# Kernel tuning notes

Measured on AMD Instinct MI355X. Metric: run time of the kernel, lower is better.

## Reference

```python
import jax, jax.numpy as jnp
import numpy as np

B, S, D = 4, 1024, 1024
H, G = 16, 8            # num_heads, num_query_groups
HD = D // H             # head_dim = 64
E, TOPK, ED = 8, 2, 2 * D   # experts, top_k, expert_dim
GH = D // 2             # gate hidden
EPS = 1e-5


def setup_inputs() -> dict:
    key = jax.random.key(0)
    ks = iter(jax.random.split(key, 32))
    rn = lambda shape, s=0.02: jax.random.normal(next(ks), shape, jnp.float32) * s
    return {
        "x": jax.random.normal(next(ks), (B, S, D), jnp.float32),
        # GQA projections (stored [in, out])
        "wq": rn((D, G * HD)), "bq": jnp.zeros((G * HD,), jnp.float32),
        "wk": rn((D, D)), "bk": jnp.zeros((D,), jnp.float32),
        "wv": rn((D, D)), "bv": jnp.zeros((D,), jnp.float32),
        "wo": rn((D, D)), "bo": jnp.zeros((D,), jnp.float32),
        # LayerNorms
        "ln1_g": jnp.ones((D,), jnp.float32), "ln1_b": jnp.zeros((D,), jnp.float32),
        "ln2_g": jnp.ones((D,), jnp.float32), "ln2_b": jnp.zeros((D,), jnp.float32),
        # MoE gate: Linear(D, D//2) -> ReLU -> Linear(D//2, E)
        "gw1": rn((D, GH)), "gb1": jnp.zeros((GH,), jnp.float32),
        "gw2": rn((GH, E)), "gb2": jnp.zeros((E,), jnp.float32),
        # stacked expert FFNs: Linear(D, ED) -> GELU -> Linear(ED, D)
        "ew1": rn((E, D, ED)), "eb1": jnp.zeros((E, ED), jnp.float32),
        "ew2": rn((E, ED, D)), "eb2": jnp.zeros((E, D), jnp.float32),
    }


def _layernorm(x, g, b):
    mu = jnp.mean(x, axis=-1, keepdims=True)
    var = jnp.var(x, axis=-1, keepdims=True)
    return (x - mu) * jax.lax.rsqrt(var + EPS) * g + b


def _block(x, wq, bq, wk, bk, wv, bv, wo, bo, ln1_g, ln1_b, ln2_g, ln2_b,
           gw1, gb1, gw2, gb2, ew1, eb1, ew2, eb2):
    # --- GQA self-attention (dropout is identity in eval) ---
    h = _layernorm(x, ln1_g, ln1_b)
    q = (h @ wq + bq).reshape(B, S, G, HD).transpose(0, 2, 1, 3)   # [B,G,S,hd]
    k = (h @ wk + bk).reshape(B, S, H, HD).transpose(0, 2, 1, 3)   # [B,H,S,hd]
    v = (h @ wv + bv).reshape(B, S, H, HD).transpose(0, 2, 1, 3)
    q = jnp.repeat(q, H // G, axis=1)                              # repeat_interleave -> [B,H,S,hd]
    scores = jnp.einsum("bhqd,bhkd->bhqk", q, k) * (HD ** -0.5)
    attn = jax.nn.softmax(scores, axis=-1)
    ao = jnp.einsum("bhqk,bhkd->bhqd", attn, v)
    ao = ao.transpose(0, 2, 1, 3).reshape(B, S, D) @ wo + bo
    x = x + ao

    # --- MoE FFN ---
    h2 = _layernorm(x, ln2_g, ln2_b).reshape(-1, D)                # [T,D], T=B*S
    gate_logits = jax.nn.relu(h2 @ gw1 + gb1) @ gw2 + gb2          # [T,E]
    gate_w = jax.nn.softmax(gate_logits, axis=-1)
    top_w, top_i = jax.lax.top_k(gate_w, TOPK)                     # [T,k]
    top_w = jax.nn.softmax(top_w, axis=-1)                         # renormalize among top-k
    combine = jnp.sum(jax.nn.one_hot(top_i, E, dtype=h2.dtype) * top_w[..., None], axis=1)  # [T,E]
    hid = jax.nn.gelu(jnp.einsum("td,edh->teh", h2, ew1) + eb1, approximate=False)          # [T,E,ED]
    expert_out = jnp.einsum("teh,ehd->ted", hid, ew2) + eb2        # [T,E,D]
    moe = jnp.einsum("ted,te->td", expert_out, combine).reshape(B, S, D)
    return x + moe


def reference(x, wq, bq, wk, bk, wv, bv, wo, bo, ln1_g, ln1_b, ln2_g, ln2_b,
              gw1, gb1, gw2, gb2, ew1, eb1, ew2, eb2):
    return _block(x, wq, bq, wk, bk, wv, bv, wo, bo, ln1_g, ln1_b, ln2_g, ln2_b,
                  gw1, gb1, gw2, gb2, ew1, eb1, ew2, eb2)
```

## Files before the change

### kernel.cpp

```cpp
#include <hip/hip_runtime.h>

typedef __bf16 bf16x8 __attribute__((ext_vector_type(8)));
typedef float f32x4 __attribute__((ext_vector_type(4)));
typedef unsigned int u32x4 __attribute__((ext_vector_type(4)));
typedef unsigned int u32x2 __attribute__((ext_vector_type(2)));

#define DEV static __device__ __forceinline__

DEV unsigned short f2bf(float f) {
  unsigned int u = __builtin_bit_cast(unsigned int, f);
  u += 0x7fffu + ((u >> 16) & 1u);
  return (unsigned short)(u >> 16);
}
DEV float bf2f(unsigned int hbits) { return __builtin_bit_cast(float, hbits << 16); }

DEV bf16x8 load_bf8(const unsigned short* p) {
  u32x4 u = *(const u32x4*)p;
  return __builtin_bit_cast(bf16x8, u);
}
DEV void unpack8(u32x4 u, float f[8]) {
  f[0] = bf2f(u.x & 0xffffu); f[1] = bf2f(u.x >> 16);
  f[2] = bf2f(u.y & 0xffffu); f[3] = bf2f(u.y >> 16);
  f[4] = bf2f(u.z & 0xffffu); f[5] = bf2f(u.z >> 16);
  f[6] = bf2f(u.w & 0xffffu); f[7] = bf2f(u.w >> 16);
}
DEV void gload_lds16(const void* g, void* l) {
  __builtin_amdgcn_global_load_lds((const __attribute__((address_space(1))) void*)g,
                                   (__attribute__((address_space(3))) void*)l, 16, 0, 0);
}
DEV f32x4 mfma16(bf16x8 a, bf16x8 b, f32x4 c) {
  return __builtin_amdgcn_mfma_f32_16x16x32_bf16(a, b, c, 0, 0, 0);
}

__global__ __launch_bounds__(256) void cm_transpose(
    const float* __restrict__ src, unsigned short* __restrict__ dst,
    int K, int N, long srcStrideE, long dstStrideE) {
  src += (long)blockIdx.z * srcStrideE;
  dst += (long)blockIdx.z * dstStrideE;
  __shared__ float t[32][33];
  const int n0 = blockIdx.x * 32, k0 = blockIdx.y * 32;
  const int tx = threadIdx.x & 31, ty = threadIdx.x >> 5;
#pragma unroll
  for (int j = 0; j < 4; ++j) {
    int k = k0 + ty + j * 8, n = n0 + tx;
    if (k < K && n < N) t[ty + j * 8][tx] = src[(long)k * N + n];
  }
  __syncthreads();
#pragma unroll
  for (int j = 0; j < 4; ++j) {
    int n = n0 + ty + j * 8, k = k0 + tx;
    if (n < N && k < K) dst[(long)n * K + k] = f2bf(t[tx][ty + j * 8]);
  }
}

__global__ __launch_bounds__(256) void cm_transpose_split(
    const float* __restrict__ src, unsigned short* __restrict__ dhi,
    unsigned short* __restrict__ dlo, int K, int N) {
  __shared__ float t[32][33];
  const int n0 = blockIdx.x * 32, k0 = blockIdx.y * 32;
  const int tx = threadIdx.x & 31, ty = threadIdx.x >> 5;
#pragma unroll
  for (int j = 0; j < 4; ++j) {
    int k = k0 + ty + j * 8, n = n0 + tx;
    if (k < K && n < N) t[ty + j * 8][tx] = src[(long)k * N + n];
  }
  __syncthreads();
#pragma unroll
  for (int j = 0; j < 4; ++j) {
    int n = n0 + ty + j * 8, k = k0 + tx;
    if (n < N && k < K) {
      float v = t[tx][ty + j * 8];
      unsigned short hi = f2bf(v);
      dhi[(long)n * K + k] = hi;
      dlo[(long)n * K + k] = f2bf(v - bf2f(hi));
    }
  }
}

template <bool WLO>
__global__ __launch_bounds__(256) void cm_ln(
    const float* __restrict__ x, const float* __restrict__ g, const float* __restrict__ b,
    unsigned short* __restrict__ ob, unsigned short* __restrict__ olo) {
  const int row = blockIdx.x, tid = threadIdx.x;
  const f32x4 v = *(const f32x4*)(x + (long)row * 1024 + tid * 4);
  float s1 = v[0] + v[1] + v[2] + v[3];
  float s2 = v[0] * v[0] + v[1] * v[1] + v[2] * v[2] + v[3] * v[3];
#pragma unroll
  for (int m = 32; m >= 1; m >>= 1) { s1 += __shfl_xor(s1, m); s2 += __shfl_xor(s2, m); }
  __shared__ float r1[4], r2[4];
  if ((tid & 63) == 0) { r1[tid >> 6] = s1; r2[tid >> 6] = s2; }
  __syncthreads();
  s1 = r1[0] + r1[1] + r1[2] + r1[3];
  s2 = r2[0] + r2[1] + r2[2] + r2[3];
  const float mean = s1 * (1.f / 1024.f);
  const float rs = rsqrtf(s2 * (1.f / 1024.f) - mean * mean + 1e-5f);
  const f32x4 gg = *(const f32x4*)(g + tid * 4);
  const f32x4 bb = *(const f32x4*)(b + tid * 4);
  float o[4];
  unsigned short hi[4];
#pragma unroll
  for (int i = 0; i < 4; ++i) {
    o[i] = (v[i] - mean) * rs * gg[i] + bb[i];
    hi[i] = f2bf(o[i]);
  }
  u32x2 pk;
  pk.x = (unsigned)hi[0] | ((unsigned)hi[1] << 16);
  pk.y = (unsigned)hi[2] | ((unsigned)hi[3] << 16);
  *(u32x2*)(ob + (long)row * 1024 + tid * 4) = pk;
  if (WLO) {
    u32x2 pl;
    pl.x = (unsigned)f2bf(o[0] - bf2f(hi[0])) | ((unsigned)f2bf(o[1] - bf2f(hi[1])) << 16);
    pl.y = (unsigned)f2bf(o[2] - bf2f(hi[2])) | ((unsigned)f2bf(o[3] - bf2f(hi[3])) << 16);
    *(u32x2*)(olo + (long)row * 1024 + tid * 4) = pl;
  }
}

enum { EP_BF16 = 0, EP_RELU = 1, EP_GELU = 2, EP_RES_F32 = 3 };

template <int EPI, int MODE>
__global__ __launch_bounds__(256, 2) void cm_gemm_bt(
    const unsigned short* __restrict__ A, int lda,
    const unsigned short* __restrict__ BT, long btStrideE, int ldb,
    const float* __restrict__ bias, int biasStrideE,
    const float* __restrict__ res,
    void* __restrict__ outp, int ldc,
    int M, int K,
    const int* __restrict__ cnt, const int* __restrict__ offs,
    const int* __restrict__ rowidx) {
  const int gx = gridDim.x, gy = gridDim.y;
  const int nwg = gx * gy * (int)gridDim.z;
  int flat = (int)blockIdx.x + gx * ((int)blockIdx.y + gy * (int)blockIdx.z);
  {
    const int q = nwg >> 3, r = nwg & 7, xcd = flat & 7, idx = flat >> 3;
    flat = (xcd < r ? xcd * (q + 1) : r * (q + 1) + (xcd - r) * q) + idx;
  }
  const int bx = flat % gx;
  const int rest = flat / gx;
  const int by = rest % gy;
  const int z = rest / gy;

  int valid = M, rowbase = 0;
  const unsigned short* Bp = BT;
  const float* biasp = bias;
  if (MODE > 0) {
    valid = cnt[z];
    if (by * 128 >= valid) return;
    rowbase = offs[z];
    Bp += (long)z * btStrideE;
    biasp += (long)z * biasStrideE;
  }
  const int tid = threadIdx.x;
  const int brow = by * 128, bcol = bx * 128;
  const int wid = tid >> 6, lane = tid & 63;
  const int wr = wid >> 1, wc = wid & 1;
  const int srow0 = tid >> 2, scol = (tid & 3) * 8;

  __shared__ __align__(16) unsigned short As[128 * 32];
  __shared__ __align__(16) unsigned short Bs[128 * 32];

  long asrc[2], bsrc[2];
#pragma unroll
  for (int i = 0; i < 2; ++i) {
    int m = brow + srow0 + i * 64;
    if (MODE == 0) {
      asrc[i] = (long)m * lda;
    } else {
      int p = m < valid ? m : valid - 1;
      if (MODE == 1) asrc[i] = (long)rowidx[z * 4096 + p] * lda;
      else           asrc[i] = (long)(rowbase + p) * lda;
    }
    bsrc[i] = (long)(bcol + srow0 + i * 64) * ldb;
  }

  f32x4 acc[4][4] = {};

  for (int k0 = 0; k0 < K; k0 += 32) {
#pragma unroll
    for (int i = 0; i < 2; ++i) {
      gload_lds16(A + asrc[i] + k0 + scol, &As[(srow0 + i * 64) * 32 + scol]);
      gload_lds16(Bp + bsrc[i] + k0 + scol, &Bs[(srow0 + i * 64) * 32 + scol]);
    }
    __syncthreads();
    bf16x8 af[4], bfr[4];
#pragma unroll
    for (int m = 0; m < 4; ++m)
      af[m] = load_bf8(&As[(wr * 64 + m * 16 + (lane & 15)) * 32 + (lane >> 4) * 8]);
#pragma unroll
    for (int n = 0; n < 4; ++n)
      bfr[n] = load_bf8(&Bs[(wc * 64 + n * 16 + (lane & 15)) * 32 + (lane >> 4) * 8]);
#pragma unroll
    for (int m = 0; m < 4; ++m)
#pragma unroll
      for (int n = 0; n < 4; ++n)
        acc[m][n] = mfma16(af[m], bfr[n], acc[m][n]);
    __syncthreads();
  }

#pragma unroll
  for (int m = 0; m < 4; ++m) {
#pragma unroll
    for (int rr = 0; rr < 4; ++rr) {
      const int lrow = brow + wr * 64 + m * 16 + (lane >> 4) * 4 + rr;
      if (MODE > 0 && lrow >= valid) continue;
      const long orow = (long)(rowbase + lrow);
#pragma unroll
      for (int n = 0; n < 4; ++n) {
        const int gcol = bcol + wc * 64 + n * 16 + (lane & 15);
        float vv = acc[m][n][rr] + biasp[gcol];
        if constexpr (EPI == EP_RELU) vv = fmaxf(vv, 0.f);
        if constexpr (EPI == EP_GELU) vv = 0.5f * vv * (1.f + erff(vv * 0.70710678f));
        if constexpr (EPI == EP_RES_F32)
          ((float*)outp)[orow * ldc + gcol] = vv + res[orow * ldc + gcol];
        else
          ((unsigned short*)outp)[orow * ldc + gcol] = f2bf(vv);
      }
    }
  }
}

__global__ __launch_bounds__(256, 2) void cm_gemm_gate(
    const unsigned short* __restrict__ Ah, const unsigned short* __restrict__ Al,
    const unsigned short* __restrict__ Bh, const unsigned short* __restrict__ Bl,
    const float* __restrict__ bias, float* __restrict__ C) {
  const int tid = threadIdx.x;
  const int brow = blockIdx.y * 128, bcol = blockIdx.x * 128;
  const int wid = tid >> 6, lane = tid & 63;
  const int wr = wid >> 1, wc = wid & 1;
  const int srow0 = tid >> 2, scol = (tid & 3) * 8;

  __shared__ __align__(16) unsigned short Ash[128 * 32], Asl[128 * 32];
  __shared__ __align__(16) unsigned short Bsh[128 * 32], Bsl[128 * 32];

  f32x4 acc[4][4] = {};

  for (int k0 = 0; k0 < 1024; k0 += 32) {
#pragma unroll
    for (int i = 0; i < 2; ++i) {
      const long ar = (long)(brow + srow0 + i * 64) * 1024 + k0 + scol;
      const long br = (long)(bcol + srow0 + i * 64) * 1024 + k0 + scol;
      const int lo = (srow0 + i * 64) * 32 + scol;
      gload_lds16(Ah + ar, &Ash[lo]);
      gload_lds16(Al + ar, &Asl[lo]);
      gload_lds16(Bh + br, &Bsh[lo]);
      gload_lds16(Bl + br, &Bsl[lo]);
    }
    __syncthreads();
    bf16x8 ah[4], al[4], bh[4], bl[4];
#pragma unroll
    for (int m = 0; m < 4; ++m) {
      const int ro = (wr * 64 + m * 16 + (lane & 15)) * 32 + (lane >> 4) * 8;
      ah[m] = load_bf8(&Ash[ro]); al[m] = load_bf8(&Asl[ro]);
    }
#pragma unroll
    for (int n = 0; n < 4; ++n) {
      const int ro = (wc * 64 + n * 16 + (lane & 15)) * 32 + (lane >> 4) * 8;
      bh[n] = load_bf8(&Bsh[ro]); bl[n] = load_bf8(&Bsl[ro]);
    }
#pragma unroll
    for (int m = 0; m < 4; ++m)
#pragma unroll
      for (int n = 0; n < 4; ++n) {
        acc[m][n] = mfma16(al[m], bh[n], acc[m][n]);
        acc[m][n] = mfma16(ah[m], bl[n], acc[m][n]);
        acc[m][n] = mfma16(ah[m], bh[n], acc[m][n]);
      }
    __syncthreads();
  }

#pragma unroll
  for (int m = 0; m < 4; ++m)
#pragma unroll
    for (int rr = 0; rr < 4; ++rr) {
      const long orow = brow + wr * 64 + m * 16 + (lane >> 4) * 4 + rr;
#pragma unroll
      for (int n = 0; n < 4; ++n) {
        const int gcol = bcol + wc * 64 + n * 16 + (lane & 15);
        C[orow * 512 + gcol] = fmaxf(acc[m][n][rr] + bias[gcol], 0.f);
      }
    }
}

__global__ __launch_bounds__(256) void cm_vtrans(
    const unsigned short* __restrict__ qkv, unsigned short* __restrict__ Vt) {
  const int stile = blockIdx.x, bh = blockIdx.y;
  const int b = bh >> 4, h = bh & 15;
  const int tid = threadIdx.x;
  __shared__ __align__(16) unsigned short t[64][72];
  const int d0 = (tid & 7) * 8, sl = tid >> 3;
#pragma unroll
  for (int i = 0; i < 2; ++i) {
    const int s = sl + i * 32;
    *(u32x4*)&t[s][d0] =
        *(const u32x4*)(qkv + (long)(b * 1024 + stile * 64 + s) * 2560 + 1536 + h * 64 + d0);
  }
  __syncthreads();
  const int s0 = (tid & 7) * 8, dl = tid >> 3;
#pragma unroll
  for (int i = 0; i < 2; ++i) {
    const int d = dl + i * 32;
    unsigned short vals[8];
#pragma unroll
    for (int j = 0; j < 8; ++j) vals[j] = t[s0 + j][d];
    u32x4 u;
    u.x = vals[0] | ((unsigned)vals[1] << 16);
    u.y = vals[2] | ((unsigned)vals[3] << 16);
    u.z = vals[4] | ((unsigned)vals[5] << 16);
    u.w = vals[6] | ((unsigned)vals[7] << 16);
    *(u32x4*)(Vt + (long)(bh * 64 + d) * 1024 + stile * 64 + s0) = u;
  }
}

__global__ __launch_bounds__(256, 2) void cm_attn(
    const unsigned short* __restrict__ qkv,
    const unsigned short* __restrict__ Vt,
    unsigned short* __restrict__ ao) {
  const int qt = blockIdx.x, bh = blockIdx.y;
  const int b = bh >> 4, h = bh & 15, g = h >> 1;
  const int tid = threadIdx.x, wid = tid >> 6, lane = tid & 63;
  const int q0 = qt * 32;

  __shared__ __align__(16) unsigned short sc[32][1032];
  __shared__ float rowrcp[32];

  bf16x8 bq[2][2];
#pragma unroll
  for (int nf = 0; nf < 2; ++nf)
#pragma unroll
    for (int ks = 0; ks < 2; ++ks)
      bq[nf][ks] = load_bf8(qkv + (long)(b * 1024 + q0 + nf * 16 + (lane & 15)) * 2560 +
                            g * 64 + ks * 32 + (lane >> 4) * 8);

#pragma unroll 1
  for (int c = 0; c < 4; ++c) {
    const int kb = wid * 256 + c * 64;
    f32x4 acc[4][2] = {};
#pragma unroll
    for (int ks = 0; ks < 2; ++ks) {
      bf16x8 ak[4];
#pragma unroll
      for (int mf = 0; mf < 4; ++mf)
        ak[mf] = load_bf8(qkv + (long)(b * 1024 + kb + mf * 16 + (lane & 15)) * 2560 +
                          512 + h * 64 + ks * 32 + (lane >> 4) * 8);
#pragma unroll
      for (int mf = 0; mf < 4; ++mf)
#pragma unroll
        for (int nf = 0; nf < 2; ++nf)
          acc[mf][nf] = mfma16(ak[mf], bq[nf][ks], acc[mf][nf]);
    }
#pragma unroll
    for (int mf = 0; mf < 4; ++mf)
#pragma unroll
      for (int nf = 0; nf < 2; ++nf) {
        const int q = nf * 16 + (lane & 15);
        const int key = kb + mf * 16 + (lane >> 4) * 4;
        u32x2 pk;
        pk.x = (unsigned)f2bf(acc[mf][nf][0] * 0.125f) |
               ((unsigned)f2bf(acc[mf][nf][1] * 0.125f) << 16);
        pk.y = (unsigned)f2bf(acc[mf][nf][2] * 0.125f) |
               ((unsigned)f2bf(acc[mf][nf][3] * 0.125f) << 16);
        *(u32x2*)&sc[q][key] = pk;
      }
  }
  __syncthreads();

  {
    const int row = tid >> 3, seg = tid & 7;
    float mx = -1e30f;
#pragma unroll
    for (int i = 0; i < 16; ++i) {
      float f[8];
      unpack8(*(const u32x4*)&sc[row][i * 64 + seg * 8], f);
#pragma unroll
      for (int j = 0; j < 8; ++j) mx = fmaxf(mx, f[j]);
    }
#pragma unroll
    for (int m = 4; m >= 1; m >>= 1) mx = fmaxf(mx, __shfl_xor(mx, m));
    float sum = 0.f;
#pragma unroll 1
    for (int i = 0; i < 16; ++i) {
      float f[8];
      unpack8(*(const u32x4*)&sc[row][i * 64 + seg * 8], f);
      float e[8];
#pragma unroll
      for (int j = 0; j < 8; ++j) { e[j] = __expf(f[j] - mx); sum += e[j]; }
      u32x4 o;
      o.x = (unsigned)f2bf(e[0]) | ((unsigned)f2bf(e[1]) << 16);
      o.y = (unsigned)f2bf(e[2]) | ((unsigned)f2bf(e[3]) << 16);
      o.z = (unsigned)f2bf(e[4]) | ((unsigned)f2bf(e[5]) << 16);
      o.w = (unsigned)f2bf(e[6]) | ((unsigned)f2bf(e[7]) << 16);
      *(u32x4*)&sc[row][i * 64 + seg * 8] = o;
    }
#pragma unroll
    for (int m = 4; m >= 1; m >>= 1) sum += __shfl_xor(sum, m);
    if (seg == 0) rowrcp[row] = 1.f / sum;
  }
  __syncthreads();

  {
    f32x4 acc[2] = {};
    const unsigned short* vtb = Vt + (long)bh * 64 * 1024;
#pragma unroll 4
    for (int k0 = 0; k0 < 1024; k0 += 32) {
      const bf16x8 bv =
          load_bf8(vtb + (long)(wid * 16 + (lane & 15)) * 1024 + k0 + (lane >> 4) * 8);
#pragma unroll
      for (int m = 0; m < 2; ++m) {
        const bf16x8 ap = load_bf8(&sc[m * 16 + (lane & 15)][k0 + (lane >> 4) * 8]);
        acc[m] = mfma16(ap, bv, acc[m]);
      }
    }
#pragma unroll
    for (int m = 0; m < 2; ++m)
#pragma unroll
      for (int rr = 0; rr < 4; ++rr) {
        const int q = m * 16 + (lane >> 4) * 4 + rr;
        const int d = wid * 16 + (lane & 15);
        ao[(long)(b * 1024 + q0 + q) * 1024 + h * 64 + d] = f2bf(acc[m][rr] * rowrcp[q]);
      }
  }
}

__global__ __launch_bounds__(64) void cm_route_pick(
    const float* __restrict__ g1f, const float* __restrict__ gw2, const float* __restrict__ gb2,
    int* __restrict__ pick, int* __restrict__ slot_e, float* __restrict__ rwt) {
  const int t = blockIdx.x, lane = threadIdx.x;
  f32x4 a0 = *(const f32x4*)(g1f + (long)t * 512 + lane * 8);
  f32x4 a1 = *(const f32x4*)(g1f + (long)t * 512 + lane * 8 + 4);
  float logit[8];
#pragma unroll
  for (int e = 0; e < 8; ++e) {
    float s = 0.f;
#pragma unroll
    for (int j = 0; j < 4; ++j) {
      s += a0[j] * gw2[(lane * 8 + j) * 8 + e];
      s += a1[j] * gw2[(lane * 8 + 4 + j) * 8 + e];
    }
#pragma unroll
    for (int m = 32; m >= 1; m >>= 1) s += __shfl_xor(s, m);
    logit[e] = s + gb2[e];
  }
  float mx = logit[0];
#pragma unroll
  for (int e = 1; e < 8; ++e) mx = fmaxf(mx, logit[e]);
  float p[8], sum = 0.f;
#pragma unroll
  for (int e = 0; e < 8; ++e) { p[e] = __expf(logit[e] - mx); sum += p[e]; }
  const float rs = 1.f / sum;
#pragma unroll
  for (int e = 0; e < 8; ++e) p[e] *= rs;
  int i0 = 0;
#pragma unroll
  for (int e = 1; e < 8; ++e) if (p[e] > p[i0]) i0 = e;
  int i1 = (i0 == 0) ? 1 : 0;
#pragma unroll
  for (int e = 0; e < 8; ++e) if (e != i0 && p[e] > p[i1]) i1 = e;
  const float w0 = 1.f / (1.f + __expf(p[i1] - p[i0]));
  if (lane == 0) {
    pick[t] = i0 | (i1 << 8);
    slot_e[t * 2] = i0; slot_e[t * 2 + 1] = i1;
    rwt[t * 2] = w0;    rwt[t * 2 + 1] = 1.f - w0;
  }
}

__global__ __launch_bounds__(256) void cm_route_place(
    const int* __restrict__ pick, int* __restrict__ cnt,
    int* __restrict__ etok, int* __restrict__ slot_p) {
  const int t = blockIdx.x * 256 + threadIdx.x;
  const int lane = threadIdx.x & 63;
  const int pk = pick[t];
  const int p0 = pk & 15, p1 = (pk >> 8) & 15;
  const unsigned long long lt = ((unsigned long long)1 << lane) - 1;
  int my_r0 = 0, my_c0p1 = 0, my_r1 = 0, tot = 0;
#pragma unroll
  for (int e = 0; e < 8; ++e) {
    const unsigned long long m0 = __ballot(p0 == e);
    const unsigned long long m1 = __ballot(p1 == e);
    if (p0 == e) my_r0 = __popcll(m0 & lt);
    if (p1 == e) { my_c0p1 = __popcll(m0); my_r1 = __popcll(m1 & lt); }
    if (lane == e) tot = __popcll(m0) + __popcll(m1);
  }
  int base = 0;
  if (lane < 8 && tot > 0) base = atomicAdd(&cnt[lane], tot);
  const int b0 = __shfl(base, p0);
  const int b1 = __shfl(base, p1);
  const int pos0 = b0 + my_r0;
  const int pos1 = b1 + my_c0p1 + my_r1;
  etok[p0 * 4096 + pos0] = t;
  etok[p1 * 4096 + pos1] = t;
  slot_p[t * 2] = pos0;
  slot_p[t * 2 + 1] = pos1;
}

__global__ void cm_offs(const int* __restrict__ cnt, int* __restrict__ offs) {
  if (threadIdx.x == 0) {
    int s = 0;
#pragma unroll
    for (int e = 0; e < 8; ++e) { offs[e] = s; s += cnt[e]; }
  }
}

__global__ __launch_bounds__(256) void cm_combine(
    const float* __restrict__ x2, const unsigned short* __restrict__ eo,
    const int* __restrict__ slot_e, const int* __restrict__ slot_p,
    const float* __restrict__ rwt, const int* __restrict__ offs,
    float* __restrict__ outp) {
  const int t = blockIdx.x, tid = threadIdx.x;
  const long r0 = (long)(offs[slot_e[t * 2]] + slot_p[t * 2]);
  const long r1 = (long)(offs[slot_e[t * 2 + 1]] + slot_p[t * 2 + 1]);
  const float w0 = rwt[t * 2], w1 = rwt[t * 2 + 1];
  const f32x4 xv = *(const f32x4*)(x2 + (long)t * 1024 + tid * 4);
  u32x2 u0 = *(const u32x2*)(eo + r0 * 1024 + tid * 4);
  u32x2 u1 = *(const u32x2*)(eo + r1 * 1024 + tid * 4);
  f32x4 o;
  o[0] = xv[0] + w0 * bf2f(u0.x & 0xffffu) + w1 * bf2f(u1.x & 0xffffu);
  o[1] = xv[1] + w0 * bf2f(u0.x >> 16) + w1 * bf2f(u1.x >> 16);
  o[2] = xv[2] + w0 * bf2f(u0.y & 0xffffu) + w1 * bf2f(u1.y & 0xffffu);
  o[3] = xv[3] + w0 * bf2f(u0.y >> 16) + w1 * bf2f(u1.y >> 16);
  *(f32x4*)(outp + (long)t * 1024 + tid * 4) = o;
}

extern "C" void kernel_launch(void* const* d_in, const int* in_sizes, int n_in,
                              void* d_out, int out_size, void* d_ws, size_t ws_size,
                              hipStream_t stream) {
  if (n_in < 21) return;
  const float* x    = (const float*)d_in[0];
  const float* wq   = (const float*)d_in[1];
  const float* bq   = (const float*)d_in[2];
  const float* wk   = (const float*)d_in[3];
  const float* bk   = (const float*)d_in[4];
  const float* wv   = (const float*)d_in[5];
  const float* bv   = (const float*)d_in[6];
  const float* wo   = (const float*)d_in[7];
  const float* bo   = (const float*)d_in[8];
  const float* ln1g = (const float*)d_in[9];
  const float* ln1b = (const float*)d_in[10];
  const float* ln2g = (const float*)d_in[11];
  const float* ln2b = (const float*)d_in[12];
  const float* gw1  = (const float*)d_in[13];
  const float* gb1  = (const float*)d_in[14];
  const float* gw2  = (const float*)d_in[15];
  const float* gb2  = (const float*)d_in[16];
  const float* ew1  = (const float*)d_in[17];
  const float* eb1  = (const float*)d_in[18];
  const float* ew2  = (const float*)d_in[19];
  const float* eb2  = (const float*)d_in[20];
  float* outp = (float*)d_out;

  char* ws = (char*)d_ws;
  size_t off = 0;
  auto carve = [&](size_t bytes) -> char* {
    char* p = ws + off;
    off += (bytes + 255) & ~(size_t)255;
    return p;
  };
  unsigned short* wqkvT = (unsigned short*)carve(2560l * 1024 * 2);
  unsigned short* woT   = (unsigned short*)carve(1024l * 1024 * 2);
  unsigned short* gw1hT = (unsigned short*)carve(512l * 1024 * 2);
  unsigned short* gw1lT = (unsigned short*)carve(512l * 1024 * 2);
  unsigned short* ew1T  = (unsigned short*)carve(8l * 2048 * 1024 * 2);
  unsigned short* ew2T  = (unsigned short*)carve(8l * 1024 * 2048 * 2);
  float* bqkv           = (float*)carve(2560 * 4);
  unsigned short* hbuf  = (unsigned short*)carve(4096l * 1024 * 2);
  unsigned short* qkvl  = (unsigned short*)carve(4096l * 2560 * 2);
  unsigned short* Vt    = (unsigned short*)carve(4096l * 1024 * 2);
  unsigned short* ao    = (unsigned short*)carve(4096l * 1024 * 2);
  unsigned short* h2    = (unsigned short*)carve(4096l * 1024 * 2);
  unsigned short* h2lo  = (unsigned short*)carve(4096l * 1024 * 2);
  int* cnt              = (int*)carve(8 * 4);
  int* offs             = (int*)carve(8 * 4);
  int* etok             = (int*)carve(8l * 4096 * 4);
  int* slot_e           = (int*)carve(8192 * 4);
  int* slot_p           = (int*)carve(8192 * 4);
  float* rwt            = (float*)carve(8192 * 4);
  int* pick             = (int*)carve(4096 * 4);
  unsigned short* hid   = (unsigned short*)carve(8192l * 2048 * 2);
  unsigned short* eo    = (unsigned short*)carve(8192l * 1024 * 2);
  if (off > ws_size) return;
  float* x2 = outp;
  float* g1f = (float*)Vt;

  (void)hipMemsetAsync(cnt, 0, 8 * 4, stream);
  (void)hipMemcpyAsync(bqkv, (const void*)bq, 512 * 4, hipMemcpyDeviceToDevice, stream);
  (void)hipMemcpyAsync(bqkv + 512, (const void*)bk, 1024 * 4, hipMemcpyDeviceToDevice, stream);
  (void)hipMemcpyAsync(bqkv + 1536, (const void*)bv, 1024 * 4, hipMemcpyDeviceToDevice, stream);

  cm_transpose<<<dim3(16, 32, 1), 256, 0, stream>>>(wq, wqkvT, 1024, 512, 0l, 0l);
  cm_transpose<<<dim3(32, 32, 1), 256, 0, stream>>>(wk, wqkvT + 512l * 1024, 1024, 1024, 0l, 0l);
  cm_transpose<<<dim3(32, 32, 1), 256, 0, stream>>>(wv, wqkvT + 1536l * 1024, 1024, 1024, 0l, 0l);
  cm_transpose<<<dim3(32, 32, 1), 256, 0, stream>>>(wo, woT, 1024, 1024, 0l, 0l);
  cm_transpose_split<<<dim3(16, 32, 1), 256, 0, stream>>>(gw1, gw1hT, gw1lT, 1024, 512);
  cm_transpose<<<dim3(64, 32, 8), 256, 0, stream>>>(ew1, ew1T, 1024, 2048, 1024l * 2048, 2048l * 1024);
  cm_transpose<<<dim3(32, 64, 8), 256, 0, stream>>>(ew2, ew2T, 2048, 1024, 2048l * 1024, 1024l * 2048);

  cm_ln<false><<<4096, 256, 0, stream>>>(x, ln1g, ln1b, hbuf, nullptr);
  cm_gemm_bt<EP_BF16, 0><<<dim3(20, 32, 1), 256, 0, stream>>>(
      hbuf, 1024, wqkvT, 0l, 1024, bqkv, 0, nullptr, qkvl, 2560, 4096, 1024,
      nullptr, nullptr, nullptr);
  cm_vtrans<<<dim3(16, 64, 1), 256, 0, stream>>>(qkvl, Vt);
  cm_attn<<<dim3(32, 64, 1), 256, 0, stream>>>(qkvl, Vt, ao);
  cm_gemm_bt<EP_RES_F32, 0><<<dim3(8, 32, 1), 256, 0, stream>>>(
      ao, 1024, woT, 0l, 1024, bo, 0, x, x2, 1024, 4096, 1024,
      nullptr, nullptr, nullptr);
  cm_ln<true><<<4096, 256, 0, stream>>>(x2, ln2g, ln2b, h2, h2lo);

  cm_gemm_gate<<<dim3(4, 32, 1), 256, 0, stream>>>(h2, h2lo, gw1hT, gw1lT, gb1, g1f);
  cm_route_pick<<<4096, 64, 0, stream>>>(g1f, gw2, gb2, pick, slot_e, rwt);
  cm_route_place<<<16, 256, 0, stream>>>(pick, cnt, etok, slot_p);
  cm_offs<<<1, 64, 0, stream>>>(cnt, offs);

  cm_gemm_bt<EP_GELU, 1><<<dim3(16, 32, 8), 256, 0, stream>>>(
      h2, 1024, ew1T, 2048l * 1024, 1024, eb1, 2048, nullptr, hid, 2048, 4096, 1024,
      cnt, offs, etok);
  cm_gemm_bt<EP_BF16, 2><<<dim3(8, 32, 8), 256, 0, stream>>>(
      hid, 2048, ew2T, 1024l * 2048, 2048, eb2, 1024, nullptr, eo, 1024, 4096, 2048,
      cnt, offs, nullptr);
  cm_combine<<<4096, 256, 0, stream>>>(x2, eo, slot_e, slot_p, rwt, offs, outp);
}
```

Before: 494.1 us.

## Double GEMM K-tile to 64 with XOR-swizzled LDS and simpler MoE grid mapping

```diff
diff --git a/kernel.cpp b/kernel.cpp
--- a/kernel.cpp
+++ b/kernel.cpp
@@ -127,17 +127,17 @@
     int M, int K,
     const int* __restrict__ cnt, const int* __restrict__ offs,
     const int* __restrict__ rowidx) {
-  const int gx = gridDim.x, gy = gridDim.y;
-  const int nwg = gx * gy * (int)gridDim.z;
-  int flat = (int)blockIdx.x + gx * ((int)blockIdx.y + gy * (int)blockIdx.z);
-  {
+  int bx, by, z;
+  if (MODE == 0) {
+    const int gx = gridDim.x, gy = gridDim.y;
+    const int nwg = gx * gy;
+    int flat = (int)blockIdx.x + gx * (int)blockIdx.y;
     const int q = nwg >> 3, r = nwg & 7, xcd = flat & 7, idx = flat >> 3;
     flat = (xcd < r ? xcd * (q + 1) : r * (q + 1) + (xcd - r) * q) + idx;
-  }
-  const int bx = flat % gx;
-  const int rest = flat / gx;
-  const int by = rest % gy;
-  const int z = rest / gy;
+    bx = flat % gx; by = flat / gx; z = 0;
+  } else {
+    bx = blockIdx.x; by = blockIdx.y; z = blockIdx.z;
+  }
 
   int valid = M, rowbase = 0;
   const unsigned short* Bp = BT;
@@ -153,15 +153,18 @@
   const int brow = by * 128, bcol = bx * 128;
   const int wid = tid >> 6, lane = tid & 63;
   const int wr = wid >> 1, wc = wid & 1;
-  const int srow0 = tid >> 2, scol = (tid & 3) * 8;
-
-  __shared__ __align__(16) unsigned short As[128 * 32];
-  __shared__ __align__(16) unsigned short Bs[128 * 32];
-
-  long asrc[2], bsrc[2];
-#pragma unroll
-  for (int i = 0; i < 2; ++i) {
-    int m = brow + srow0 + i * 64;
+
+  const int srow = tid >> 3, sc = tid & 7;
+  const int scg = ((sc ^ (srow & 7)) << 3);
+  const int ldst = srow * 64 + sc * 8;
+
+  __shared__ __align__(16) unsigned short As[128 * 64];
+  __shared__ __align__(16) unsigned short Bs[128 * 64];
+
+  long asrc[4], bsrc[4];
+#pragma unroll
+  for (int i = 0; i < 4; ++i) {
+    int m = brow + srow + i * 32;
     if (MODE == 0) {
       asrc[i] = (long)m * lda;
     } else {
@@ -169,30 +172,37 @@
       if (MODE == 1) asrc[i] = (long)rowidx[z * 4096 + p] * lda;
       else           asrc[i] = (long)(rowbase + p) * lda;
     }
-    bsrc[i] = (long)(bcol + srow0 + i * 64) * ldb;
+    bsrc[i] = (long)(bcol + srow + i * 32) * ldb;
   }
 
   f32x4 acc[4][4] = {};
 
-  for (int k0 = 0; k0 < K; k0 += 32) {
-#pragma unroll
-    for (int i = 0; i < 2; ++i) {
-      gload_lds16(A + asrc[i] + k0 + scol, &As[(srow0 + i * 64) * 32 + scol]);
-      gload_lds16(Bp + bsrc[i] + k0 + scol, &Bs[(srow0 + i * 64) * 32 + scol]);
+  for (int k0 = 0; k0 < K; k0 += 64) {
+#pragma unroll
+    for (int i = 0; i < 4; ++i) {
+      gload_lds16(A + asrc[i] + k0 + scg, &As[ldst + i * 2048]);
+      gload_lds16(Bp + bsrc[i] + k0 + scg, &Bs[ldst + i * 2048]);
     }
     __syncthreads();
-    bf16x8 af[4], bfr[4];
-#pragma unroll
-    for (int m = 0; m < 4; ++m)
-      af[m] = load_bf8(&As[(wr * 64 + m * 16 + (lane & 15)) * 32 + (lane >> 4) * 8]);
-#pragma unroll
-    for (int n = 0; n < 4; ++n)
-      bfr[n] = load_bf8(&Bs[(wc * 64 + n * 16 + (lane & 15)) * 32 + (lane >> 4) * 8]);
-#pragma unroll
-    for (int m = 0; m < 4; ++m)
-#pragma unroll
-      for (int n = 0; n < 4; ++n)
-        acc[m][n] = mfma16(af[m], bfr[n], acc[m][n]);
+#pragma unroll
+    for (int ks = 0; ks < 2; ++ks) {
+      bf16x8 af[4], bfr[4];
+#pragma unroll
+      for (int m = 0; m < 4; ++m) {
+        const int r = wr * 64 + m * 16 + (lane & 15);
+        af[m] = load_bf8(&As[r * 64 + (((ks * 4 + (lane >> 4)) ^ (lane & 7)) << 3)]);
+      }
+#pragma unroll
+      for (int n = 0; n < 4; ++n) {
+        const int r = wc * 64 + n * 16 + (lane & 15);
+        bfr[n] = load_bf8(&Bs[r * 64 + (((ks * 4 + (lane >> 4)) ^ (lane & 7)) << 3)]);
+      }
+#pragma unroll
+      for (int m = 0; m < 4; ++m)
+#pragma unroll
+        for (int n = 0; n < 4; ++n)
+          acc[m][n] = mfma16(af[m], bfr[n], acc[m][n]);
+    }
     __syncthreads();
   }
 
```

New measurement: 449.6 us. -9.0%, faster.
